# Performance work log

Hardware: AMD Instinct MI355X
Metric: run time of the kernel (lower is better)

The kernel has to match this reference:

```python
import jax, jax.numpy as jnp
import numpy as np

BS, C, D = 4096, 16384, 128
POS_ALPHA, POS_DELTA = 32.0, 0.1
NEG_ALPHA, NEG_DELTA = 32.0, -0.1


def _normalize(x):
    # F.normalize(x, dim=1)
    return x / jnp.linalg.norm(x, axis=1, keepdims=True)


def _masked_lse(sims, mask, axis, use_max):
    """Faithful port of Criterion.masked_logsumexp (returns per-entry lse and the
    nonzero-entry mask that torch uses to filter before the final mean)."""
    m = sims * mask
    if use_max:
        ref = jnp.max(m, axis=axis, keepdims=True)
    else:
        ref = jnp.min(m, axis=axis, keepdims=True)
    ref = jax.lax.stop_gradient(ref)  # torch: ref_v.detach()
    # torch: nz_entries = max + min of (sims*mask); keep where nonzero
    nz = (jnp.max(m, axis=axis) + jnp.min(m, axis=axis)) != 0
    s = jnp.sum(jnp.exp(sims - ref) * mask, axis=axis)
    lse = jnp.log(jnp.where(nz, s, 1.0)) + jnp.squeeze(ref, axis=axis)
    return lse, nz


def setup_inputs() -> dict:
    key = jax.random.key(0)
    k1, k2, k3 = jax.random.split(key, 3)
    batch = jax.random.normal(k1, (BS, D), dtype=jnp.float32)
    # proxies = randn/proxy_div, init_dev=0 so no max-shift
    proxies = jax.random.normal(k2, (C, D), dtype=jnp.float32) / 8.0
    labels = jax.random.randint(k3, (BS,), 0, C)
    return {"batch": batch, "proxies": proxies, "labels": labels}


def reference(batch, proxies, labels):
    batch = _normalize(batch)          # [BS, D]
    proxies = _normalize(proxies)      # [C, D]

    pos_sims = batch @ proxies[labels].T   # [BS, BS] cosine sims to positive proxies
    sims = batch @ proxies.T               # [BS, C]

    same = (labels[:, None] == labels[None, :]).astype(batch.dtype)              # [BS, BS]
    diff = (labels[:, None] != jnp.arange(C)[None, :]).astype(batch.dtype)       # [BS, C]

    w_pos = -POS_ALPHA * (pos_sims - POS_DELTA)
    w_neg = NEG_ALPHA * (sims - NEG_DELTA)

    # mode='anchor' -> dim=0; cosine -> max=False for pos, max=True for neg
    pos_lse, pos_nz = _masked_lse(w_pos, same, axis=0, use_max=False)
    neg_lse, neg_nz = _masked_lse(w_neg, diff, axis=0, use_max=True)

    # nca_clean=False -> softplus
    pos_s = jax.nn.softplus(pos_lse)
    neg_s = jax.nn.softplus(neg_lse)

    # torch takes mean only over nz entries
    pos_mean = jnp.sum(jnp.where(pos_nz, pos_s, 0.0)) / jnp.maximum(jnp.sum(pos_nz), 1).astype(batch.dtype)
    neg_mean = jnp.sum(jnp.where(neg_nz, neg_s, 0.0)) / jnp.maximum(jnp.sum(neg_nz), 1).astype(batch.dtype)
    return pos_mean + neg_mean
```

## Files before the change

kernel.cpp:

```cpp
#include <hip/hip_runtime.h>
#include <math.h>

#define BS 4096
#define C_CLS 16384
#define D 128
#define NS 8
#define NR 8
#define KE 46.16624130844683f
#define POS_C 4.616624130844683f
#define LN2 0.69314718055994531f
#define CORR_BLOCKS 1024
#define NEG_BLOCKS 512

typedef __attribute__((ext_vector_type(8))) short short8;
typedef __attribute__((ext_vector_type(4))) float f32x4;

__device__ inline float bf2f(unsigned short h) {
    return __uint_as_float(((unsigned)h) << 16);
}
__device__ inline unsigned short f2bf(float f) {
    unsigned u = __float_as_uint(f);
    u += 0x7FFF + ((u >> 16) & 1);
    return (unsigned short)(u >> 16);
}
__device__ inline float fast_exp2(float x) {
#if __has_builtin(__builtin_amdgcn_exp2f)
    return __builtin_amdgcn_exp2f(x);
#else
    return exp2f(x);
#endif
}
__device__ inline float softplus(float x) {
    return fmaxf(x, 0.0f) + log1pf(__expf(-fabsf(x)));
}
__device__ inline void gload16(const void* g, void* l) {
    __builtin_amdgcn_global_load_lds((const __attribute__((address_space(1))) void*)g,
                                     (__attribute__((address_space(3))) void*)l, 16, 0, 0);
}
__device__ inline unsigned fenc(float f) {
    unsigned u = __float_as_uint(f);
    return (u & 0x80000000u) ? ~u : (u | 0x80000000u);
}
__device__ inline float fdec(unsigned k) {
    return (k & 0x80000000u) ? __uint_as_float(k ^ 0x80000000u) : __uint_as_float(~k);
}

__global__ __launch_bounds__(256) void normalize_all(const float* __restrict__ batch,
                                                     const float* __restrict__ proxies,
                                                     short* __restrict__ bbf,
                                                     short* __restrict__ pbf,
                                                     float* __restrict__ acc,
                                                     float* __restrict__ negSub,
                                                     float* __restrict__ posSum,
                                                     float* __restrict__ posCnt,
                                                     unsigned* __restrict__ posMaxK,
                                                     unsigned* __restrict__ posMinK,
                                                     int* __restrict__ counter) {
    const int w = threadIdx.x >> 6, lane = threadIdx.x & 63;
    const int row = blockIdx.x * 4 + w;
    const bool isb = row < BS;
    const float* src = isb ? batch : proxies;
    short* dst = isb ? bbf : pbf;
    const int r = isb ? row : row - BS;
    const float sc = isb ? 1.0f : KE;

    float2 v = ((const float2*)(src + (size_t)r * D))[lane];
    float ss = v.x * v.x + v.y * v.y;
#pragma unroll
    for (int off = 32; off; off >>= 1) ss += __shfl_xor(ss, off);
    float inv = rsqrtf(ss) * sc;
    ushort2 o;
    o.x = f2bf(v.x * inv);
    o.y = f2bf(v.y * inv);
    ((ushort2*)(dst + (size_t)r * D))[lane] = o;

    const int bid = blockIdx.x, t = bid * 256 + threadIdx.x;
    if (bid < 64) negSub[t] = 0.0f;
    else if (bid < 128) posSum[t - 64 * 256] = 0.0f;
    else if (bid < 192) posCnt[t - 128 * 256] = 0.0f;
    else if (bid < 256) posMaxK[t - 192 * 256] = 0u;
    else if (bid < 320) posMinK[t - 256 * 256] = 0xFFFFFFFFu;
    if (bid == 0) {
        if (threadIdx.x < 4) acc[threadIdx.x] = 0.0f;
        if (threadIdx.x == 4) *counter = 0;
    }
}

__global__ __launch_bounds__(256, 4) void mm_all(const short* __restrict__ pbf,
                                                 const short* __restrict__ bbf,
                                                 const int* __restrict__ labels,
                                                 float* __restrict__ S,
                                                 float* __restrict__ negSub,
                                                 float* __restrict__ posSum,
                                                 float* __restrict__ posCnt,
                                                 unsigned* __restrict__ posMaxK,
                                                 unsigned* __restrict__ posMinK) {
    __shared__ short8 frag[3][16 * 64];

    const int bid = blockIdx.x;
    const int tid = threadIdx.x;
    const int w = tid >> 6, lane = tid & 63, l16 = lane & 15, g = lane >> 4;

    if (bid < CORR_BLOCKS) {
        const int i = bid * 4 + w;
        const int lab = labels[i];
        ushort2 av = ((const ushort2*)(bbf + (size_t)i * D))[lane];
        ushort2 pv = ((const ushort2*)(pbf + (size_t)lab * D))[lane];
        float d = bf2f(av.x) * bf2f(pv.x) + bf2f(av.y) * bf2f(pv.y);
#pragma unroll
        for (int off = 32; off; off >>= 1) d += __shfl_xor(d, off);
        if (lane == 0) {
            atomicAdd(&negSub[lab], fast_exp2(d));
            atomicAdd(&posSum[lab], fast_exp2(POS_C - d));
            atomicAdd(&posCnt[lab], 1.0f);
            float wv = fmaf(d, -LN2, 3.2f);
            unsigned k = fenc(wv);
            atomicMax(&posMaxK[lab], k);
            atomicMin(&posMinK[lab], k);
        }
        return;
    }

    const int n = bid - CORR_BLOCKS;
    const int pg = (n & 7) * 8 + ((n >> 3) & 7);
    const int sp = n >> 6;
    const int wbase = pg * 256 + w * 64;

    short8 a[4][4];
#pragma unroll
    for (int pt = 0; pt < 4; pt++)
#pragma unroll
        for (int kk = 0; kk < 4; kk++)
            a[pt][kk] = *(const short8*)(pbf + (size_t)(wbase + pt * 16 + l16) * D + kk * 32 + g * 8);
    asm volatile("" ::: "memory");

    const int ibeg = sp * (BS / NS);
    const short* srcbase = bbf + (size_t)(ibeg + w * 16 + l16) * D + g * 8;

#define STAGE(rr)                                                            \
    {                                                                        \
        const short* sn_ = srcbase + (size_t)(rr) * 64 * D;                  \
        _Pragma("unroll") for (int kk = 0; kk < 4; kk++)                     \
            gload16(sn_ + kk * 32, &frag[(rr) % 3][(w * 4 + kk) * 64]);      \
    }

    STAGE(0)
    STAGE(1)

    float s[4][4];
#pragma unroll
    for (int pt = 0; pt < 4; pt++)
#pragma unroll
        for (int r = 0; r < 4; r++) s[pt][r] = 0.0f;

#pragma unroll
    for (int rnd = 0; rnd < NR; rnd++) {
        if (rnd < NR - 1)
            asm volatile("s_waitcnt vmcnt(4)" ::: "memory");
        else
            asm volatile("s_waitcnt vmcnt(0)" ::: "memory");
        __builtin_amdgcn_s_barrier();

        const short8* fb = &frag[rnd % 3][0];
        __builtin_amdgcn_s_setprio(1);
#pragma unroll
        for (int bt = 0; bt < 4; bt++) {
            short8 b[4];
#pragma unroll
            for (int kk = 0; kk < 4; kk++) b[kk] = fb[(bt * 4 + kk) * 64 + lane];
#pragma unroll
            for (int pt = 0; pt < 4; pt++) {
                f32x4 acc = {0.0f, 0.0f, 0.0f, 0.0f};
#pragma unroll
                for (int kk = 0; kk < 4; kk++)
                    acc = __builtin_amdgcn_mfma_f32_16x16x32_bf16(a[pt][kk], b[kk], acc, 0, 0, 0);
#pragma unroll
                for (int r = 0; r < 4; r++) s[pt][r] += fast_exp2(acc[r]);
            }
        }
        __builtin_amdgcn_s_setprio(0);

        if (rnd + 2 < NR) STAGE(rnd + 2)
    }
#undef STAGE

#pragma unroll
    for (int off = 1; off < 16; off <<= 1)
#pragma unroll
        for (int pt = 0; pt < 4; pt++)
#pragma unroll
            for (int r = 0; r < 4; r++) s[pt][r] += __shfl_xor(s[pt][r], off);

    if (l16 == 0) {
#pragma unroll
        for (int pt = 0; pt < 4; pt++)
#pragma unroll
            for (int r = 0; r < 4; r++) {
                int row = wbase + pt * 16 + g * 4 + r;
                S[(size_t)sp * C_CLS + row] = s[pt][r];
            }
    }
}

__global__ __launch_bounds__(256) void final_reduce(const float* __restrict__ S,
                                                    const float* __restrict__ negSub,
                                                    const int* __restrict__ labels,
                                                    const float* __restrict__ posSum,
                                                    const float* __restrict__ posCnt,
                                                    const unsigned* __restrict__ posMaxK,
                                                    const unsigned* __restrict__ posMinK,
                                                    float* __restrict__ acc,
                                                    int* __restrict__ counter,
                                                    float* __restrict__ out) {
    const int n = blockIdx.x * 256 + threadIdx.x;
    float add = 0.0f, cnt = 0.0f;
    int slot;
    if (n < C_CLS) {
        slot = 2;
        float s = 0.0f;
#pragma unroll
        for (int p = 0; p < NS; p++) s += S[(size_t)p * C_CLS + n];
        s = fmaxf(s - negSub[n], 1e-30f);
        add = softplus(logf(s) + 3.2f);
        cnt = 1.0f;
    } else {
        slot = 0;
        const int j = n - C_CLS;
        const int lab = labels[j];
        float s = posSum[lab], c = posCnt[lab];
        float mxw = fdec(posMaxK[lab]), mnw = fdec(posMinK[lab]);
        float maxm = (c < (float)BS) ? fmaxf(mxw, 0.0f) : mxw;
        float minm = (c < (float)BS) ? fminf(mnw, 0.0f) : mnw;
        bool nz = (maxm + minm) != 0.0f;
        if (nz) {
            add = softplus(logf(s));
            cnt = 1.0f;
        }
    }
#pragma unroll
    for (int off = 32; off; off >>= 1) {
        add += __shfl_xor(add, off);
        cnt += __shfl_xor(cnt, off);
    }
    if ((threadIdx.x & 63) == 0) {
        atomicAdd(&acc[slot], add);
        atomicAdd(&acc[slot + 1], cnt);
    }

    __shared__ int amLast;
    __threadfence();
    if (threadIdx.x == 0) amLast = (atomicAdd(counter, 1) == (int)gridDim.x - 1);
    __syncthreads();
    if (amLast && threadIdx.x == 0) {
        __threadfence();
        out[0] = acc[0] / fmaxf(acc[1], 1.0f) + acc[2] / fmaxf(acc[3], 1.0f);
    }
}

extern "C" void kernel_launch(void* const* d_in, const int* in_sizes, int n_in,
                              void* d_out, int out_size, void* d_ws, size_t ws_size,
                              hipStream_t stream) {
    const float* batch = (const float*)d_in[0];
    const float* proxies = (const float*)d_in[1];
    const int* labels = (const int*)d_in[2];
    float* out = (float*)d_out;

    char* ws = (char*)d_ws;
    float* acc = (float*)ws;
    int* counter = (int*)(ws + 64);
    short* bbf = (short*)(ws + 256);
    short* pbf = (short*)(ws + 256 + (size_t)BS * D * 2);
    char* p = ws + 256 + (size_t)(BS + C_CLS) * D * 2;
    float* negS = (float*)p;       p += (size_t)C_CLS * NS * 4;
    float* negSub = (float*)p;     p += (size_t)C_CLS * 4;
    float* posSum = (float*)p;     p += (size_t)C_CLS * 4;
    float* posCnt = (float*)p;     p += (size_t)C_CLS * 4;
    unsigned* posMaxK = (unsigned*)p; p += (size_t)C_CLS * 4;
    unsigned* posMinK = (unsigned*)p;

    normalize_all<<<(BS + C_CLS) / 4, 256, 0, stream>>>(batch, proxies, bbf, pbf, acc,
                                                        negSub, posSum, posCnt, posMaxK,
                                                        posMinK, counter);
    mm_all<<<CORR_BLOCKS + NEG_BLOCKS, 256, 0, stream>>>(pbf, bbf, labels, negS, negSub,
                                                         posSum, posCnt, posMaxK, posMinK);
    final_reduce<<<(C_CLS + BS) / 256, 256, 0, stream>>>(negS, negSub, labels, posSum,
                                                         posCnt, posMaxK, posMinK,
                                                         acc, counter, out);
}
```

Measured before the change: 53.47 us.

## Split negative-sim GEMM into more smaller blocks with double buffering and vectorized normalize

The negative-similarity kernel now launches 2048 blocks instead of 512. Each wave handles 32 proxy rows instead of 64, and the batch is split into 16 slices instead of 8. The three-stage LDS ring becomes a two-buffer scheme with a full wait and an extra barrier per round, and a 5-blocks-per-CU launch bound. The negative blocks are placed before the correlation blocks, and the normalize kernel now handles 8 rows per block using float4 loads. The aim is better CU occupancy and load balance for the exp-bound inner loop, at the cost of less proxy-fragment reuse, more partial sums to reduce, and weaker load/compute overlap.

```diff
diff --git a/kernel.cpp b/kernel.cpp
--- a/kernel.cpp
+++ b/kernel.cpp
@@ -4,13 +4,13 @@
 #define BS 4096
 #define C_CLS 16384
 #define D 128
-#define NS 8
-#define NR 8
+#define NS 16
+#define NR 4
 #define KE 46.16624130844683f
 #define POS_C 4.616624130844683f
 #define LN2 0.69314718055994531f
+#define NEG_BLOCKS 2048
 #define CORR_BLOCKS 1024
-#define NEG_BLOCKS 512
 
 typedef __attribute__((ext_vector_type(8))) short short8;
 typedef __attribute__((ext_vector_type(4))) float f32x4;
@@ -56,23 +56,26 @@
                                                      unsigned* __restrict__ posMaxK,
                                                      unsigned* __restrict__ posMinK,
                                                      int* __restrict__ counter) {
-    const int w = threadIdx.x >> 6, lane = threadIdx.x & 63;
-    const int row = blockIdx.x * 4 + w;
+    const int sub = threadIdx.x >> 5;
+    const int lane32 = threadIdx.x & 31;
+    const int row = blockIdx.x * 8 + sub;
     const bool isb = row < BS;
     const float* src = isb ? batch : proxies;
     short* dst = isb ? bbf : pbf;
     const int r = isb ? row : row - BS;
     const float sc = isb ? 1.0f : KE;
 
-    float2 v = ((const float2*)(src + (size_t)r * D))[lane];
-    float ss = v.x * v.x + v.y * v.y;
-#pragma unroll
-    for (int off = 32; off; off >>= 1) ss += __shfl_xor(ss, off);
+    float4 v = ((const float4*)(src + (size_t)r * D))[lane32];
+    float ss = v.x * v.x + v.y * v.y + v.z * v.z + v.w * v.w;
+#pragma unroll
+    for (int off = 16; off; off >>= 1) ss += __shfl_xor(ss, off);
     float inv = rsqrtf(ss) * sc;
-    ushort2 o;
+    ushort4 o;
     o.x = f2bf(v.x * inv);
     o.y = f2bf(v.y * inv);
-    ((ushort2*)(dst + (size_t)r * D))[lane] = o;
+    o.z = f2bf(v.z * inv);
+    o.w = f2bf(v.w * inv);
+    ((ushort4*)(dst + (size_t)r * D))[lane32] = o;
 
     const int bid = blockIdx.x, t = bid * 256 + threadIdx.x;
     if (bid < 64) negSub[t] = 0.0f;
@@ -86,7 +89,7 @@
     }
 }
 
-__global__ __launch_bounds__(256, 4) void mm_all(const short* __restrict__ pbf,
+__global__ __launch_bounds__(256, 5) void mm_all(const short* __restrict__ pbf,
                                                  const short* __restrict__ bbf,
                                                  const int* __restrict__ labels,
                                                  float* __restrict__ S,
@@ -95,14 +98,14 @@
                                                  float* __restrict__ posCnt,
                                                  unsigned* __restrict__ posMaxK,
                                                  unsigned* __restrict__ posMinK) {
-    __shared__ short8 frag[3][16 * 64];
+    __shared__ short8 frag[2][16 * 64];
 
     const int bid = blockIdx.x;
     const int tid = threadIdx.x;
     const int w = tid >> 6, lane = tid & 63, l16 = lane & 15, g = lane >> 4;
 
-    if (bid < CORR_BLOCKS) {
-        const int i = bid * 4 + w;
+    if (bid >= NEG_BLOCKS) {
+        const int i = (bid - NEG_BLOCKS) * 4 + w;
         const int lab = labels[i];
         ushort2 av = ((const ushort2*)(bbf + (size_t)i * D))[lane];
         ushort2 pv = ((const ushort2*)(pbf + (size_t)lab * D))[lane];
@@ -121,18 +124,11 @@
         return;
     }
 
-    const int n = bid - CORR_BLOCKS;
-    const int pg = (n & 7) * 8 + ((n >> 3) & 7);
-    const int sp = n >> 6;
-    const int wbase = pg * 256 + w * 64;
-
-    short8 a[4][4];
-#pragma unroll
-    for (int pt = 0; pt < 4; pt++)
-#pragma unroll
-        for (int kk = 0; kk < 4; kk++)
-            a[pt][kk] = *(const short8*)(pbf + (size_t)(wbase + pt * 16 + l16) * D + kk * 32 + g * 8);
-    asm volatile("" ::: "memory");
+    const int n = bid;
+    const int idx = n >> 3;
+    const int pg = (n & 7) * 16 + (idx & 15);
+    const int sp = idx >> 4;
+    const int wbase = pg * 128 + w * 32;
 
     const int ibeg = sp * (BS / NS);
     const short* srcbase = bbf + (size_t)(ibeg + w * 16 + l16) * D + g * 8;
@@ -141,27 +137,31 @@
     {                                                                        \
         const short* sn_ = srcbase + (size_t)(rr) * 64 * D;                  \
         _Pragma("unroll") for (int kk = 0; kk < 4; kk++)                     \
-            gload16(sn_ + kk * 32, &frag[(rr) % 3][(w * 4 + kk) * 64]);      \
+            gload16(sn_ + kk * 32, &frag[(rr) & 1][(w * 4 + kk) * 64]);      \
     }
 
     STAGE(0)
-    STAGE(1)
-
-    float s[4][4];
-#pragma unroll
-    for (int pt = 0; pt < 4; pt++)
+
+    short8 a[2][4];
+#pragma unroll
+    for (int pt = 0; pt < 2; pt++)
+#pragma unroll
+        for (int kk = 0; kk < 4; kk++)
+            a[pt][kk] = *(const short8*)(pbf + (size_t)(wbase + pt * 16 + l16) * D + kk * 32 + g * 8);
+
+    float s[2][4];
+#pragma unroll
+    for (int pt = 0; pt < 2; pt++)
 #pragma unroll
         for (int r = 0; r < 4; r++) s[pt][r] = 0.0f;
 
 #pragma unroll
     for (int rnd = 0; rnd < NR; rnd++) {
-        if (rnd < NR - 1)
-            asm volatile("s_waitcnt vmcnt(4)" ::: "memory");
-        else
-            asm volatile("s_waitcnt vmcnt(0)" ::: "memory");
+        asm volatile("s_waitcnt vmcnt(0)" ::: "memory");
         __builtin_amdgcn_s_barrier();
-
-        const short8* fb = &frag[rnd % 3][0];
+        if (rnd + 1 < NR) STAGE(rnd + 1)
+
+        const short8* fb = &frag[rnd & 1][0];
         __builtin_amdgcn_s_setprio(1);
 #pragma unroll
         for (int bt = 0; bt < 4; bt++) {
@@ -169,7 +169,7 @@
 #pragma unroll
             for (int kk = 0; kk < 4; kk++) b[kk] = fb[(bt * 4 + kk) * 64 + lane];
 #pragma unroll
-            for (int pt = 0; pt < 4; pt++) {
+            for (int pt = 0; pt < 2; pt++) {
                 f32x4 acc = {0.0f, 0.0f, 0.0f, 0.0f};
 #pragma unroll
                 for (int kk = 0; kk < 4; kk++)
@@ -179,21 +179,20 @@
             }
         }
         __builtin_amdgcn_s_setprio(0);
-
-        if (rnd + 2 < NR) STAGE(rnd + 2)
+        __builtin_amdgcn_s_barrier();
     }
 #undef STAGE
 
 #pragma unroll
     for (int off = 1; off < 16; off <<= 1)
 #pragma unroll
-        for (int pt = 0; pt < 4; pt++)
+        for (int pt = 0; pt < 2; pt++)
 #pragma unroll
             for (int r = 0; r < 4; r++) s[pt][r] += __shfl_xor(s[pt][r], off);
 
     if (l16 == 0) {
 #pragma unroll
-        for (int pt = 0; pt < 4; pt++)
+        for (int pt = 0; pt < 2; pt++)
 #pragma unroll
             for (int r = 0; r < 4; r++) {
                 int row = wbase + pt * 16 + g * 4 + r;
@@ -278,10 +277,10 @@
     unsigned* posMaxK = (unsigned*)p; p += (size_t)C_CLS * 4;
     unsigned* posMinK = (unsigned*)p;
 
-    normalize_all<<<(BS + C_CLS) / 4, 256, 0, stream>>>(batch, proxies, bbf, pbf, acc,
+    normalize_all<<<(BS + C_CLS) / 8, 256, 0, stream>>>(batch, proxies, bbf, pbf, acc,
                                                         negSub, posSum, posCnt, posMaxK,
                                                         posMinK, counter);
-    mm_all<<<CORR_BLOCKS + NEG_BLOCKS, 256, 0, stream>>>(pbf, bbf, labels, negS, negSub,
+    mm_all<<<NEG_BLOCKS + CORR_BLOCKS, 256, 0, stream>>>(pbf, bbf, labels, negS, negSub,
                                                          posSum, posCnt, posMaxK, posMinK);
     final_reduce<<<(C_CLS + BS) / 256, 256, 0, stream>>>(negS, negSub, labels, posSum,
                                                          posCnt, posMaxK, posMinK,
```

Result: slower. 78.35 us (+46.5%).
